# Optimization experiments

Hardware: AMD Instinct MI355X
Metric: run time of the kernel (lower is better)

## Reference

```python
import jax, jax.numpy as jnp
import numpy as np

C = 1.0          # curvature
KP_EXTENT = 0.66 # kernel point influence radius
N, NEI, K, DIN, DOUT = 20000, 16, 4, 64, 64


def _artanh(x):
    return jnp.arctanh(jnp.clip(x, -1.0 + 1e-7, 1.0 - 1e-7))

def _norm(x):
    return jnp.sqrt(jnp.clip(jnp.sum(x * x, -1, keepdims=True), 1e-14))

def _proj(x, c=C):
    n = _norm(x)
    maxn = (1.0 - 1e-5) / jnp.sqrt(c)
    return jnp.where(n > maxn, x / n * maxn, x)

def _expmap0(u, c=C):
    sc = jnp.sqrt(c)
    n = _norm(u)
    return jnp.tanh(sc * n) * u / (sc * n)

def _logmap0(p, c=C):
    sc = jnp.sqrt(c)
    n = _norm(p)
    return _artanh(sc * n) * p / (sc * n)

def _mobius_add(x, y, c=C):
    x2 = jnp.sum(x * x, -1, keepdims=True)
    y2 = jnp.sum(y * y, -1, keepdims=True)
    xy = jnp.sum(x * y, -1, keepdims=True)
    num = (1 + 2 * c * xy + c * y2) * x + (1 - c * x2) * y
    den = jnp.clip(1 + 2 * c * xy + c * c * x2 * y2, 1e-15)
    return num / den

def _lambda_x(x, c=C):
    return 2.0 / jnp.clip(1 - c * jnp.sum(x * x, -1, keepdims=True), 1e-7)

def _dist(x, y, c=C):  # sqrt(sqdist)
    sc = jnp.sqrt(c)
    m = _mobius_add(-x, y, c)
    return (2.0 / sc) * _artanh(sc * _norm(m)[..., 0])

def _logmap(x, y, c=C):
    m = _mobius_add(-x, y, c)
    n = _norm(m)
    sc = jnp.sqrt(c)
    return 2.0 / (sc * _lambda_x(x, c)) * _artanh(sc * n) * m / n

def _ptransp0back(x, u, c=C):  # parallel transport x -> origin
    return u * _lambda_x(x, c) / 2.0

def _p2k(x, c=C):  # Poincare -> Klein
    return 2.0 * x / (1 + c * jnp.sum(x * x, -1, keepdims=True))

def _k2p(x, c=C):  # Klein -> Poincare
    return x / (1 + jnp.sqrt(jnp.clip(1 - c * jnp.sum(x * x, -1, keepdims=True), 1e-7)))

def _gamma(x, c=C):  # Lorentz factor of a Klein point
    return 1.0 / jnp.sqrt(jnp.clip(1 - c * jnp.sum(x * x, -1, keepdims=True), 1e-7))


def setup_inputs() -> dict:
    key = jax.random.key(0)
    k1, k2, k3, k4, k5 = jax.random.split(key, 5)
    x = _proj(0.1 * jax.random.normal(k1, (N, DIN), jnp.float32))   # points in the ball
    nei = jax.random.randint(k2, (N, NEI), 0, N)                    # neighbor indices
    nei_mask = jnp.ones((N, NEI), jnp.float32)
    W = jax.random.normal(k3, (K, DOUT, DIN), jnp.float32) * (2.0 / (DIN + DOUT)) ** 0.5
    b = 0.01 * jax.random.normal(k4, (K, DOUT), jnp.float32)
    kt = jax.random.normal(k5, (K, DIN), jnp.float32)
    kt = kt / _norm(kt) * KP_EXTENT                                 # tangent kernel points on radius
    kt = kt.at[0].set(0.0)                                          # center kernel point
    return {"x": x, "nei": nei, "nei_mask": nei_mask, "W": W, "b": b, "kernel_tangents": kt}


def reference(x, nei, nei_mask, W, b, kernel_tangents):
    # 1) irregular neighbor gather: (N, NEI, D)
    x_nei = x[nei]
    xr = x[:, None, :]
    # 2) transport_x: move every neighborhood to the origin
    x0_nei = _proj(_expmap0(_ptransp0back(xr, _logmap(xr, x_nei))))
    # 3) kernel positions at the origin (after transport, transp=False branch)
    x_kernel = _expmap0(kernel_tangents)                        # (K, D)
    # 4) per neighbor / kernel-point hyperbolic distances: (N, K, NEI)
    dis = _dist(x0_nei[:, None, :, :], x_kernel[None, :, None, :])
    # 5) per-kernel BLinear: log0 -> linear -> exp0 -> mobius bias add -> proj
    u = _logmap0(x0_nei)                                        # (N, NEI, D)
    h = _expmap0(jnp.einsum('kod,bnd->bkno', W, u))             # (N, K, NEI, DOUT)
    h = _proj(_mobius_add(h, _expmap0(b)[None, :, None, :]))
    # 6) KPConv linear influence weights, masked
    w = jax.nn.relu(1.0 - dis / KP_EXTENT) * nei_mask[:, None, :]
    # 7) Klein weighted midpoint over neighbors (AggKlein=True)
    kx = _p2k(h)
    wg = w * _gamma(kx)[..., 0]                                 # (N, K, NEI)
    mid = jnp.einsum('bkn,bknd->bkd', wg, kx) / jnp.clip(jnp.sum(wg, -1, keepdims=True)[..., None][..., 0, :], 1e-10)
    # 8) Klein midpoint over the K kernel points
    g = _gamma(mid)                                             # (N, K, 1)
    out_k = jnp.sum(g * mid, 1) / jnp.clip(jnp.sum(g, 1), 1e-10)
    out = _proj(_k2p(out_k))
    # 9) hyperbolic activation (BAct with relu in tangent space at origin)
    return _expmap0(jax.nn.relu(_logmap0(out)))
```

## Files before the change

kernel.cpp:

```cpp
#include <hip/hip_runtime.h>

#define NEI 16
#define KK 4
#define DIN 64
#define DOUT 64
#define WPB 4
#define BLK (WPB * 64)
#define MAXBLOCKS 2048

__device__ __forceinline__ float wave_bcast_sum(float v) {
#pragma unroll
  for (int s = 1; s < 64; s <<= 1) v += __shfl_xor(v, s, 64);
  return v;
}

__device__ __forceinline__ float artanh_c(float z) {
  z = fminf(z, 1.0f - 1e-7f);
  z = fmaxf(z, -1.0f + 1e-7f);
  return atanhf(z);
}

__device__ __forceinline__ float tanh_fast(float r) {
  const float e = __expf(2.f * r);
  return (e - 1.f) / (e + 1.f);
}

__device__ __forceinline__ float cosh_fast(float t) {
  const float e = __expf(t);
  return 0.5f * (e + 1.f / e);
}

__global__ __launch_bounds__(BLK) void kpa_fused(
    const float* __restrict__ x, const int* __restrict__ nei,
    const float* __restrict__ nmask, const float* __restrict__ Wg,
    const float* __restrict__ bias, const float* __restrict__ kt,
    float* __restrict__ out, int npts) {
  __shared__ __align__(16) float sXK[KK][DIN];
  __shared__ __align__(16) float sEB[KK][DOUT];
  __shared__ float sXK2[KK], sEB2[KK], sAT[KK];
  __shared__ __align__(16) float sUv[WPB][DIN];

  const int tid = threadIdx.x, wv = tid >> 6, lane = tid & 63;

  {
    float v = kt[wv * DIN + lane];
    float bv = bias[wv * DOUT + lane];
    float n2 = wave_bcast_sum(v * v);
    float nr = sqrtf(fmaxf(n2, 1e-14f));
    float t = tanh_fast(nr);
    sXK[wv][lane] = t / nr * v;
    float bn2 = wave_bcast_sum(bv * bv);
    float bnr = sqrtf(fmaxf(bn2, 1e-14f));
    float tb = tanh_fast(bnr);
    sEB[wv][lane] = tb / bnr * bv;
    if (lane == 0) {
      sXK2[wv] = t * t;
      sEB2[wv] = tb * tb;
      sAT[wv] = nr;
    }
  }
  __syncthreads();

  const float maxAT = fmaxf(fmaxf(sAT[0], sAT[1]), fmaxf(sAT[2], sAT[3]));
  const float Cthr = 0.5f * (cosh_fast(0.68f + 2.f * maxAT) - 1.f);

  const int nn = lane >> 2, q = lane & 3, kme = lane & 3;
  const int stride = gridDim.x * WPB;

  int b = blockIdx.x * WPB + wv;
  if (b >= npts) return;

  int jc = nei[b * NEI + nn];
  float4 yc[4], xc[4];
  {
    const float4* yr = reinterpret_cast<const float4*>(x + (size_t)jc * DIN);
    const float4* xr = reinterpret_cast<const float4*>(x + (size_t)b * DIN);
#pragma unroll
    for (int c = 0; c < 4; ++c) {
      xc[c] = xr[c * 4 + q];
      yc[c] = yr[c * 4 + q];
    }
  }
  int b1 = b + stride;
  int j1 = (b1 < npts) ? nei[b1 * NEI + nn] : 0;

  for (;;) {
    const bool hasn = (b1 < npts);

    float4 yn[4], xn[4];
    if (hasn) {
      const float4* yr = reinterpret_cast<const float4*>(x + (size_t)j1 * DIN);
      const float4* xr = reinterpret_cast<const float4*>(x + (size_t)b1 * DIN);
#pragma unroll
      for (int c = 0; c < 4; ++c) {
        xn[c] = xr[c * 4 + q];
        yn[c] = yr[c * 4 + q];
      }
    }
    const int b2 = b1 + stride;
    int j2 = 0;
    if (hasn && b2 < npts) j2 = nei[b2 * NEI + nn];
    __builtin_amdgcn_sched_barrier(0);

    float xyc[4], y2c[4], x2c[4];
#pragma unroll
    for (int c = 0; c < 4; ++c) {
      float a = yc[c].x * xc[c].x, d = yc[c].x * yc[c].x, e = xc[c].x * xc[c].x;
      a = fmaf(yc[c].y, xc[c].y, a); d = fmaf(yc[c].y, yc[c].y, d); e = fmaf(xc[c].y, xc[c].y, e);
      a = fmaf(yc[c].z, xc[c].z, a); d = fmaf(yc[c].z, yc[c].z, d); e = fmaf(xc[c].z, xc[c].z, e);
      a = fmaf(yc[c].w, xc[c].w, a); d = fmaf(yc[c].w, yc[c].w, d); e = fmaf(xc[c].w, xc[c].w, e);
      xyc[c] = a; y2c[c] = d; x2c[c] = e;
    }
    float xy = (xyc[0] + xyc[1]) + (xyc[2] + xyc[3]);
    float y2 = (y2c[0] + y2c[1]) + (y2c[2] + y2c[3]);
    float x2 = (x2c[0] + x2c[1]) + (x2c[2] + x2c[3]);
#pragma unroll
    for (int s = 1; s < 4; s <<= 1) {
      xy += __shfl_xor(xy, s, 64);
      y2 += __shfl_xor(y2, s, 64);
      x2 += __shfl_xor(x2, s, 64);
    }

    const float e2 = fmaxf(x2 - 2.f * xy + y2, 0.f);
    const bool nearp = e2 < Cthr * (1.f - x2) * (1.f - y2);

    if (__ballot(nearp) == 0ull) {
      out[(size_t)b * DOUT + lane] = 0.f;
    } else {
      const float Bc = 1.f - x2;
      const float A = 1.f - 2.f * xy + y2;
      const float den = fmaxf(1.f - 2.f * xy + x2 * y2, 1e-15f);
      const float inv = 1.f / den;
      const float num2 = fmaxf(A * A * x2 - 2.f * A * Bc * xy + Bc * Bc * y2, 0.f);
      const float nm2 = num2 * inv * inv;

      const float mskme = nmask[b * NEI + nn];
      float dk[KK] = {0.f, 0.f, 0.f, 0.f};
      float pk[KK] = {0.f, 0.f, 0.f, 0.f};
#pragma unroll
      for (int k = 0; k < KK; ++k) {
        const float4* xkp = reinterpret_cast<const float4*>(&sXK[k][0]);
#pragma unroll
        for (int c = 0; c < 4; ++c) {
          const float4 xk4 = xkp[c * 4 + q];
          dk[k] = fmaf(yc[c].x, xk4.x, dk[k]); dk[k] = fmaf(yc[c].y, xk4.y, dk[k]);
          dk[k] = fmaf(yc[c].z, xk4.z, dk[k]); dk[k] = fmaf(yc[c].w, xk4.w, dk[k]);
          pk[k] = fmaf(xc[c].x, xk4.x, pk[k]); pk[k] = fmaf(xc[c].y, xk4.y, pk[k]);
          pk[k] = fmaf(xc[c].z, xk4.z, pk[k]); pk[k] = fmaf(xc[c].w, xk4.w, pk[k]);
        }
      }
#pragma unroll
      for (int s = 1; s < 4; s <<= 1) {
#pragma unroll
        for (int k = 0; k < KK; ++k) {
          dk[k] += __shfl_xor(dk[k], s, 64);
          pk[k] += __shfl_xor(pk[k], s, 64);
        }
      }
      const float Pjme = dk[kme];
      const float Pbme = pk[kme];

      const float nmr = sqrtf(fmaxf(nm2, 1e-14f));
      const float scl = (nmr > 0.99999f) ? (0.99999f / nmr) : 1.f;
      const float fac = inv * scl;
      const float n02 = nm2 * scl * scl;
      const float B2 = 1.f - n02;
      const float dd = fac * (Bc * Pjme - A * Pbme);
      const float xk2 = sXK2[kme];
      const float A2 = 1.f - 2.f * dd + xk2;
      const float dn2 = fmaxf(1.f - 2.f * dd + n02 * xk2, 1e-15f);
      const float nu2 = fmaxf(A2 * A2 * n02 - 2.f * A2 * B2 * dd + B2 * B2 * xk2, 0.f);
      const float mm2 = nu2 / (dn2 * dn2);
      float w = 0.f;
      if (mm2 < 0.101505f && mskme > 0.f) {
        const float dis = 2.f * artanh_c(sqrtf(fmaxf(mm2, 1e-14f)));
        w = fmaxf(1.f - dis * (1.0f / 0.66f), 0.f) * mskme;
      }
      const unsigned long long act = __ballot(w > 0.f);
      if (act == 0ull) {
        out[(size_t)b * DOUT + lane] = 0.f;
      } else {
        const float xbd = x[(size_t)b * DIN + lane];
        float midv[KK];
#pragma unroll
        for (int k = 0; k < KK; ++k) {
          float macc = 0.f, wsm = 0.f;
          unsigned long long m = act & (0x1111111111111111ull << k);
          const float ebt = sEB[k][lane];
          const float eb2 = sEB2[k];
          while (m) {
            const int g = __ffsll(m) - 1;
            m &= m - 1;
            const float wn = __shfl(w, g, 64);
            const float fac_n = __shfl(fac, g, 64);
            const float A_n = __shfl(A, g, 64);
            const float n02_n = __shfl(n02, g, 64);
            const int j_n = __shfl(jc, g, 64);
            const float yd = x[(size_t)j_n * DIN + lane];
            const float x0t = fac_n * (Bc * yd - A_n * xbd);
            const float n0 = sqrtf(fmaxf(n02_n, 1e-14f));
            const float al = artanh_c(n0) / n0;
            asm volatile("s_waitcnt lgkmcnt(0)" ::: "memory");
            sUv[wv][lane] = al * x0t;
            asm volatile("s_waitcnt lgkmcnt(0)" ::: "memory");
            __builtin_amdgcn_sched_barrier(0);
            float a0 = 0.f, a1 = 0.f, a2 = 0.f, a3 = 0.f;
            const float4* wrow = reinterpret_cast<const float4*>(Wg) + ((k * DOUT + lane) << 4);
            const float4* urow = reinterpret_cast<const float4*>(&sUv[wv][0]);
#pragma unroll
            for (int g4 = 0; g4 < 16; ++g4) {
              const float4 w4 = wrow[g4];
              const float4 u4 = urow[g4];
              a0 = fmaf(w4.x, u4.x, a0);
              a1 = fmaf(w4.y, u4.y, a1);
              a2 = fmaf(w4.z, u4.z, a2);
              a3 = fmaf(w4.w, u4.w, a3);
            }
            const float hpre = (a0 + a1) + (a2 + a3);
            const float nh2 = wave_bcast_sum(hpre * hpre);
            const float nh = sqrtf(fmaxf(nh2, 1e-14f));
            const float sh = tanhf(nh) / nh;
            const float ht = sh * hpre;
            const float hx2 = sh * sh * nh2;
            const float hxy = wave_bcast_sum(ht * ebt);
            const float A3 = 1.f + 2.f * hxy + eb2;
            const float B3 = 1.f - hx2;
            const float dn3 = fmaxf(1.f + 2.f * hxy + hx2 * eb2, 1e-15f);
            float hm = (A3 * ht + B3 * ebt) / dn3;
            float n2h = wave_bcast_sum(hm * hm);
            const float nnh = sqrtf(fmaxf(n2h, 1e-14f));
            if (nnh > 0.99999f) {
              const float s = 0.99999f / nnh;
              hm *= s;
              n2h *= s * s;
            }
            const float ip = 1.f / (1.f + n2h);
            const float kx = 2.f * hm * ip;
            const float kx2 = 4.f * n2h * ip * ip;
            const float gam = 1.f / sqrtf(fmaxf(1.f - kx2, 1e-7f));
            const float wgv = wn * gam;
            macc = fmaf(wgv, kx, macc);
            wsm += wgv;
          }
          midv[k] = macc / fmaxf(wsm, 1e-10f);
        }

        float m2v[KK];
#pragma unroll
        for (int k = 0; k < KK; ++k) m2v[k] = midv[k] * midv[k];
#pragma unroll
        for (int s = 1; s < 64; s <<= 1) {
#pragma unroll
          for (int k = 0; k < KK; ++k) m2v[k] += __shfl_xor(m2v[k], s, 64);
        }
        float onum = 0.f, oden = 0.f;
#pragma unroll
        for (int k = 0; k < KK; ++k) {
          const float g = 1.f / sqrtf(fmaxf(1.f - m2v[k], 1e-7f));
          onum = fmaf(g, midv[k], onum);
          oden += g;
        }
        const float ok = onum / fmaxf(oden, 1e-10f);
        const float no2 = wave_bcast_sum(ok * ok);
        float p = ok / (1.f + sqrtf(fmaxf(1.f - no2, 1e-7f)));
        float np2 = wave_bcast_sum(p * p);
        float npn = sqrtf(fmaxf(np2, 1e-14f));
        if (npn > 0.99999f) {
          p *= 0.99999f / npn;
          npn = 0.99999f;
        }
        const float al2 = artanh_c(npn) / npn;
        const float rr = fmaxf(al2 * p, 0.f);
        const float nr2 = wave_bcast_sum(rr * rr);
        const float nrr = sqrtf(fmaxf(nr2, 1e-14f));
        out[(size_t)b * DOUT + lane] = tanhf(nrr) / nrr * rr;
      }
    }

    if (!hasn) break;
    b = b1;
    jc = j1;
    b1 = b2;
    j1 = j2;
#pragma unroll
    for (int c = 0; c < 4; ++c) {
      yc[c] = yn[c];
      xc[c] = xn[c];
    }
  }
}

extern "C" void kernel_launch(void* const* d_in, const int* in_sizes, int n_in,
                              void* d_out, int out_size, void* d_ws, size_t ws_size,
                              hipStream_t stream) {
  const float* x = (const float*)d_in[0];
  const int* nei = (const int*)d_in[1];
  const float* nmask = (const float*)d_in[2];
  const float* W = (const float*)d_in[3];
  const float* bias = (const float*)d_in[4];
  const float* kt = (const float*)d_in[5];
  float* out = (float*)d_out;

  const int npts = in_sizes[0] / DIN;
  int grid = (npts + WPB - 1) / WPB;
  if (grid > MAXBLOCKS) grid = MAXBLOCKS;
  kpa_fused<<<grid, BLK, 0, stream>>>(x, nei, nmask, W, bias, kt, out, npts);
}
```

Before: 23.33 us.

## Split into gate kernel building a worklist and a compact heavy kernel

Adds a light gate kernel that zeroes every output row, runs the cheap proximity test per point, and appends surviving point indices to a workspace worklist through an atomic counter. A second kernel with a fixed grid of 128 blocks then processes only the listed points with the full hyperbolic pipeline. The aim is to remove divergence and the idle slots that sparse active points leave in the grid-stride fused loop. In exchange it adds a memset and an extra launch, plus atomic contention. The fused kernel is kept as a fallback when no workspace is available, and its register prefetch pipelining is removed.

```diff
diff --git a/kernel.cpp b/kernel.cpp
--- a/kernel.cpp
+++ b/kernel.cpp
@@ -7,6 +7,7 @@
 #define WPB 4
 #define BLK (WPB * 64)
 #define MAXBLOCKS 2048
+#define WLOFF 64
 
 __device__ __forceinline__ float wave_bcast_sum(float v) {
 #pragma unroll
@@ -28,6 +29,265 @@
 __device__ __forceinline__ float cosh_fast(float t) {
   const float e = __expf(t);
   return 0.5f * (e + 1.f / e);
+}
+
+__global__ __launch_bounds__(BLK, 6) void kpa_gate(
+    const float* __restrict__ x, const int* __restrict__ nei,
+    const float* __restrict__ kt, float* __restrict__ out,
+    int* __restrict__ wl, int npts) {
+  __shared__ float sAT[KK];
+  const int tid = threadIdx.x, wv = tid >> 6, lane = tid & 63;
+  {
+    float v = kt[wv * DIN + lane];
+    float n2 = wave_bcast_sum(v * v);
+    if (lane == 0) sAT[wv] = sqrtf(fmaxf(n2, 1e-14f));
+  }
+  __syncthreads();
+  const float maxAT = fmaxf(fmaxf(sAT[0], sAT[1]), fmaxf(sAT[2], sAT[3]));
+  const float Cthr = 0.5f * (cosh_fast(0.68f + 2.f * maxAT) - 1.f);
+
+  const int b = blockIdx.x * WPB + wv;
+  if (b >= npts) return;
+  const int nn = lane >> 2, q = lane & 3;
+  const int j = nei[b * NEI + nn];
+
+  out[(size_t)b * DOUT + lane] = 0.f;
+
+  const float4* yr = reinterpret_cast<const float4*>(x + (size_t)j * DIN);
+  const float4* xr = reinterpret_cast<const float4*>(x + (size_t)b * DIN);
+  float xy = 0.f, y2 = 0.f, x2 = 0.f;
+#pragma unroll
+  for (int c = 0; c < 4; ++c) {
+    const float4 yv = yr[c * 4 + q];
+    const float4 xv = xr[c * 4 + q];
+    xy = fmaf(yv.x, xv.x, xy); xy = fmaf(yv.y, xv.y, xy);
+    xy = fmaf(yv.z, xv.z, xy); xy = fmaf(yv.w, xv.w, xy);
+    y2 = fmaf(yv.x, yv.x, y2); y2 = fmaf(yv.y, yv.y, y2);
+    y2 = fmaf(yv.z, yv.z, y2); y2 = fmaf(yv.w, yv.w, y2);
+    x2 = fmaf(xv.x, xv.x, x2); x2 = fmaf(xv.y, xv.y, x2);
+    x2 = fmaf(xv.z, xv.z, x2); x2 = fmaf(xv.w, xv.w, x2);
+  }
+#pragma unroll
+  for (int s = 1; s < 4; s <<= 1) {
+    xy += __shfl_xor(xy, s, 64);
+    y2 += __shfl_xor(y2, s, 64);
+    x2 += __shfl_xor(x2, s, 64);
+  }
+  const float e2 = fmaxf(x2 - 2.f * xy + y2, 0.f);
+  const bool nearp = e2 < Cthr * (1.f - x2) * (1.f - y2);
+  if (__ballot(nearp) != 0ull && lane == 0) {
+    const int idx = atomicAdd(wl, 1);
+    wl[WLOFF + idx] = b;
+  }
+}
+
+__global__ __launch_bounds__(BLK) void kpa_heavy(
+    const float* __restrict__ x, const int* __restrict__ nei,
+    const float* __restrict__ nmask, const float* __restrict__ Wg,
+    const float* __restrict__ bias, const float* __restrict__ kt,
+    const int* __restrict__ wl, float* __restrict__ out, int npts) {
+  __shared__ __align__(16) float sXK[KK][DIN];
+  __shared__ __align__(16) float sEB[KK][DOUT];
+  __shared__ float sXK2[KK], sEB2[KK];
+  __shared__ __align__(16) float sUv[WPB][DIN];
+
+  const int tid = threadIdx.x, wv = tid >> 6, lane = tid & 63;
+  {
+    float v = kt[wv * DIN + lane];
+    float bv = bias[wv * DOUT + lane];
+    float n2 = wave_bcast_sum(v * v);
+    float nr = sqrtf(fmaxf(n2, 1e-14f));
+    float t = tanh_fast(nr);
+    sXK[wv][lane] = t / nr * v;
+    float bn2 = wave_bcast_sum(bv * bv);
+    float bnr = sqrtf(fmaxf(bn2, 1e-14f));
+    float tb = tanh_fast(bnr);
+    sEB[wv][lane] = tb / bnr * bv;
+    if (lane == 0) {
+      sXK2[wv] = t * t;
+      sEB2[wv] = tb * tb;
+    }
+  }
+  __syncthreads();
+
+  const int cnt = wl[0];
+  const int nn = lane >> 2, q = lane & 3, kme = lane & 3;
+  const int stride = gridDim.x * WPB;
+
+  for (int i = blockIdx.x * WPB + wv; i < cnt; i += stride) {
+    const int b = wl[WLOFF + i];
+    const int jc = nei[b * NEI + nn];
+    const float mskme = nmask[b * NEI + nn];
+
+    float4 yc[4], xc[4];
+    {
+      const float4* yr = reinterpret_cast<const float4*>(x + (size_t)jc * DIN);
+      const float4* xr = reinterpret_cast<const float4*>(x + (size_t)b * DIN);
+#pragma unroll
+      for (int c = 0; c < 4; ++c) {
+        xc[c] = xr[c * 4 + q];
+        yc[c] = yr[c * 4 + q];
+      }
+    }
+    float xy = 0.f, y2 = 0.f, x2 = 0.f;
+    float dk[KK] = {0.f, 0.f, 0.f, 0.f};
+    float pk[KK] = {0.f, 0.f, 0.f, 0.f};
+#pragma unroll
+    for (int c = 0; c < 4; ++c) {
+      xy = fmaf(yc[c].x, xc[c].x, xy); xy = fmaf(yc[c].y, xc[c].y, xy);
+      xy = fmaf(yc[c].z, xc[c].z, xy); xy = fmaf(yc[c].w, xc[c].w, xy);
+      y2 = fmaf(yc[c].x, yc[c].x, y2); y2 = fmaf(yc[c].y, yc[c].y, y2);
+      y2 = fmaf(yc[c].z, yc[c].z, y2); y2 = fmaf(yc[c].w, yc[c].w, y2);
+      x2 = fmaf(xc[c].x, xc[c].x, x2); x2 = fmaf(xc[c].y, xc[c].y, x2);
+      x2 = fmaf(xc[c].z, xc[c].z, x2); x2 = fmaf(xc[c].w, xc[c].w, x2);
+    }
+#pragma unroll
+    for (int k = 0; k < KK; ++k) {
+      const float4* xkp = reinterpret_cast<const float4*>(&sXK[k][0]);
+#pragma unroll
+      for (int c = 0; c < 4; ++c) {
+        const float4 xk4 = xkp[c * 4 + q];
+        dk[k] = fmaf(yc[c].x, xk4.x, dk[k]); dk[k] = fmaf(yc[c].y, xk4.y, dk[k]);
+        dk[k] = fmaf(yc[c].z, xk4.z, dk[k]); dk[k] = fmaf(yc[c].w, xk4.w, dk[k]);
+        pk[k] = fmaf(xc[c].x, xk4.x, pk[k]); pk[k] = fmaf(xc[c].y, xk4.y, pk[k]);
+        pk[k] = fmaf(xc[c].z, xk4.z, pk[k]); pk[k] = fmaf(xc[c].w, xk4.w, pk[k]);
+      }
+    }
+#pragma unroll
+    for (int s = 1; s < 4; s <<= 1) {
+      xy += __shfl_xor(xy, s, 64);
+      y2 += __shfl_xor(y2, s, 64);
+      x2 += __shfl_xor(x2, s, 64);
+#pragma unroll
+      for (int k = 0; k < KK; ++k) {
+        dk[k] += __shfl_xor(dk[k], s, 64);
+        pk[k] += __shfl_xor(pk[k], s, 64);
+      }
+    }
+
+    const float Bc = 1.f - x2;
+    const float A = 1.f - 2.f * xy + y2;
+    const float den = fmaxf(1.f - 2.f * xy + x2 * y2, 1e-15f);
+    const float inv = 1.f / den;
+    const float num2 = fmaxf(A * A * x2 - 2.f * A * Bc * xy + Bc * Bc * y2, 0.f);
+    const float nm2 = num2 * inv * inv;
+    const float nmr = sqrtf(fmaxf(nm2, 1e-14f));
+    const float scl = (nmr > 0.99999f) ? (0.99999f / nmr) : 1.f;
+    const float fac = inv * scl;
+    const float n02 = nm2 * scl * scl;
+    const float B2 = 1.f - n02;
+    const float dd = fac * (Bc * dk[kme] - A * pk[kme]);
+    const float xk2 = sXK2[kme];
+    const float A2 = 1.f - 2.f * dd + xk2;
+    const float dn2 = fmaxf(1.f - 2.f * dd + n02 * xk2, 1e-15f);
+    const float nu2 = fmaxf(A2 * A2 * n02 - 2.f * A2 * B2 * dd + B2 * B2 * xk2, 0.f);
+    const float mm2 = nu2 / (dn2 * dn2);
+    float w = 0.f;
+    if (mm2 < 0.101505f && mskme > 0.f) {
+      const float dis = 2.f * artanh_c(sqrtf(fmaxf(mm2, 1e-14f)));
+      w = fmaxf(1.f - dis * (1.0f / 0.66f), 0.f) * mskme;
+    }
+    const unsigned long long act = __ballot(w > 0.f);
+    if (act == 0ull) {
+      out[(size_t)b * DOUT + lane] = 0.f;
+      continue;
+    }
+
+    const float xbd = x[(size_t)b * DIN + lane];
+    float midv[KK];
+#pragma unroll
+    for (int k = 0; k < KK; ++k) {
+      float macc = 0.f, wsm = 0.f;
+      unsigned long long m = act & (0x1111111111111111ull << k);
+      const float ebt = sEB[k][lane];
+      const float eb2 = sEB2[k];
+      while (m) {
+        const int g = __ffsll(m) - 1;
+        m &= m - 1;
+        const float wn = __shfl(w, g, 64);
+        const float fac_n = __shfl(fac, g, 64);
+        const float A_n = __shfl(A, g, 64);
+        const float n02_n = __shfl(n02, g, 64);
+        const int j_n = __shfl(jc, g, 64);
+        const float yd = x[(size_t)j_n * DIN + lane];
+        const float x0t = fac_n * (Bc * yd - A_n * xbd);
+        const float n0 = sqrtf(fmaxf(n02_n, 1e-14f));
+        const float al = artanh_c(n0) / n0;
+        asm volatile("s_waitcnt lgkmcnt(0)" ::: "memory");
+        sUv[wv][lane] = al * x0t;
+        asm volatile("s_waitcnt lgkmcnt(0)" ::: "memory");
+        __builtin_amdgcn_sched_barrier(0);
+        float a0 = 0.f, a1 = 0.f, a2 = 0.f, a3 = 0.f;
+        const float4* wrow = reinterpret_cast<const float4*>(Wg) + ((k * DOUT + lane) << 4);
+        const float4* urow = reinterpret_cast<const float4*>(&sUv[wv][0]);
+#pragma unroll
+        for (int g4 = 0; g4 < 16; ++g4) {
+          const float4 w4 = wrow[g4];
+          const float4 u4 = urow[g4];
+          a0 = fmaf(w4.x, u4.x, a0);
+          a1 = fmaf(w4.y, u4.y, a1);
+          a2 = fmaf(w4.z, u4.z, a2);
+          a3 = fmaf(w4.w, u4.w, a3);
+        }
+        const float hpre = (a0 + a1) + (a2 + a3);
+        const float nh2 = wave_bcast_sum(hpre * hpre);
+        const float nh = sqrtf(fmaxf(nh2, 1e-14f));
+        const float sh = tanhf(nh) / nh;
+        const float ht = sh * hpre;
+        const float hx2 = sh * sh * nh2;
+        const float hxy = wave_bcast_sum(ht * ebt);
+        const float A3 = 1.f + 2.f * hxy + eb2;
+        const float B3 = 1.f - hx2;
+        const float dn3 = fmaxf(1.f + 2.f * hxy + hx2 * eb2, 1e-15f);
+        float hm = (A3 * ht + B3 * ebt) / dn3;
+        float n2h = wave_bcast_sum(hm * hm);
+        const float nnh = sqrtf(fmaxf(n2h, 1e-14f));
+        if (nnh > 0.99999f) {
+          const float s = 0.99999f / nnh;
+          hm *= s;
+          n2h *= s * s;
+        }
+        const float ip = 1.f / (1.f + n2h);
+        const float kx = 2.f * hm * ip;
+        const float kx2 = 4.f * n2h * ip * ip;
+        const float gam = 1.f / sqrtf(fmaxf(1.f - kx2, 1e-7f));
+        const float wgv = wn * gam;
+        macc = fmaf(wgv, kx, macc);
+        wsm += wgv;
+      }
+      midv[k] = macc / fmaxf(wsm, 1e-10f);
+    }
+
+    float m2v[KK];
+#pragma unroll
+    for (int k = 0; k < KK; ++k) m2v[k] = midv[k] * midv[k];
+#pragma unroll
+    for (int s = 1; s < 64; s <<= 1) {
+#pragma unroll
+      for (int k = 0; k < KK; ++k) m2v[k] += __shfl_xor(m2v[k], s, 64);
+    }
+    float onum = 0.f, oden = 0.f;
+#pragma unroll
+    for (int k = 0; k < KK; ++k) {
+      const float g = 1.f / sqrtf(fmaxf(1.f - m2v[k], 1e-7f));
+      onum = fmaf(g, midv[k], onum);
+      oden += g;
+    }
+    const float ok = onum / fmaxf(oden, 1e-10f);
+    const float no2 = wave_bcast_sum(ok * ok);
+    float p = ok / (1.f + sqrtf(fmaxf(1.f - no2, 1e-7f)));
+    float np2 = wave_bcast_sum(p * p);
+    float npn = sqrtf(fmaxf(np2, 1e-14f));
+    if (npn > 0.99999f) {
+      p *= 0.99999f / npn;
+      npn = 0.99999f;
+    }
+    const float al2 = artanh_c(npn) / npn;
+    const float rr = fmaxf(al2 * p, 0.f);
+    const float nr2 = wave_bcast_sum(rr * rr);
+    const float nrr = sqrtf(fmaxf(nr2, 1e-14f));
+    out[(size_t)b * DOUT + lane] = tanhf(nrr) / nrr * rr;
+  }
 }
 
 __global__ __launch_bounds__(BLK) void kpa_fused(
@@ -41,7 +301,6 @@
   __shared__ __align__(16) float sUv[WPB][DIN];
 
   const int tid = threadIdx.x, wv = tid >> 6, lane = tid & 63;
-
   {
     float v = kt[wv * DIN + lane];
     float bv = bias[wv * DOUT + lane];
@@ -63,230 +322,186 @@
 
   const float maxAT = fmaxf(fmaxf(sAT[0], sAT[1]), fmaxf(sAT[2], sAT[3]));
   const float Cthr = 0.5f * (cosh_fast(0.68f + 2.f * maxAT) - 1.f);
-
   const int nn = lane >> 2, q = lane & 3, kme = lane & 3;
   const int stride = gridDim.x * WPB;
 
-  int b = blockIdx.x * WPB + wv;
-  if (b >= npts) return;
-
-  int jc = nei[b * NEI + nn];
-  float4 yc[4], xc[4];
-  {
-    const float4* yr = reinterpret_cast<const float4*>(x + (size_t)jc * DIN);
-    const float4* xr = reinterpret_cast<const float4*>(x + (size_t)b * DIN);
+  for (int b = blockIdx.x * WPB + wv; b < npts; b += stride) {
+    const int jc = nei[b * NEI + nn];
+    float4 yc[4], xc[4];
+    {
+      const float4* yr = reinterpret_cast<const float4*>(x + (size_t)jc * DIN);
+      const float4* xr = reinterpret_cast<const float4*>(x + (size_t)b * DIN);
+#pragma unroll
+      for (int c = 0; c < 4; ++c) {
+        xc[c] = xr[c * 4 + q];
+        yc[c] = yr[c * 4 + q];
+      }
+    }
+    float xy = 0.f, y2 = 0.f, x2 = 0.f;
 #pragma unroll
     for (int c = 0; c < 4; ++c) {
-      xc[c] = xr[c * 4 + q];
-      yc[c] = yr[c * 4 + q];
-    }
-  }
-  int b1 = b + stride;
-  int j1 = (b1 < npts) ? nei[b1 * NEI + nn] : 0;
-
-  for (;;) {
-    const bool hasn = (b1 < npts);
-
-    float4 yn[4], xn[4];
-    if (hasn) {
-      const float4* yr = reinterpret_cast<const float4*>(x + (size_t)j1 * DIN);
-      const float4* xr = reinterpret_cast<const float4*>(x + (size_t)b1 * DIN);
-#pragma unroll
-      for (int c = 0; c < 4; ++c) {
-        xn[c] = xr[c * 4 + q];
-        yn[c] = yr[c * 4 + q];
-      }
-    }
-    const int b2 = b1 + stride;
-    int j2 = 0;
-    if (hasn && b2 < npts) j2 = nei[b2 * NEI + nn];
-    __builtin_amdgcn_sched_barrier(0);
-
-    float xyc[4], y2c[4], x2c[4];
-#pragma unroll
-    for (int c = 0; c < 4; ++c) {
-      float a = yc[c].x * xc[c].x, d = yc[c].x * yc[c].x, e = xc[c].x * xc[c].x;
-      a = fmaf(yc[c].y, xc[c].y, a); d = fmaf(yc[c].y, yc[c].y, d); e = fmaf(xc[c].y, xc[c].y, e);
-      a = fmaf(yc[c].z, xc[c].z, a); d = fmaf(yc[c].z, yc[c].z, d); e = fmaf(xc[c].z, xc[c].z, e);
-      a = fmaf(yc[c].w, xc[c].w, a); d = fmaf(yc[c].w, yc[c].w, d); e = fmaf(xc[c].w, xc[c].w, e);
-      xyc[c] = a; y2c[c] = d; x2c[c] = e;
-    }
-    float xy = (xyc[0] + xyc[1]) + (xyc[2] + xyc[3]);
-    float y2 = (y2c[0] + y2c[1]) + (y2c[2] + y2c[3]);
-    float x2 = (x2c[0] + x2c[1]) + (x2c[2] + x2c[3]);
+      xy = fmaf(yc[c].x, xc[c].x, xy); xy = fmaf(yc[c].y, xc[c].y, xy);
+      xy = fmaf(yc[c].z, xc[c].z, xy); xy = fmaf(yc[c].w, xc[c].w, xy);
+      y2 = fmaf(yc[c].x, yc[c].x, y2); y2 = fmaf(yc[c].y, yc[c].y, y2);
+      y2 = fmaf(yc[c].z, yc[c].z, y2); y2 = fmaf(yc[c].w, yc[c].w, y2);
+      x2 = fmaf(xc[c].x, xc[c].x, x2); x2 = fmaf(xc[c].y, xc[c].y, x2);
+      x2 = fmaf(xc[c].w, xc[c].w, x2); x2 = fmaf(xc[c].z, xc[c].z, x2);
+    }
 #pragma unroll
     for (int s = 1; s < 4; s <<= 1) {
       xy += __shfl_xor(xy, s, 64);
       y2 += __shfl_xor(y2, s, 64);
       x2 += __shfl_xor(x2, s, 64);
     }
-
     const float e2 = fmaxf(x2 - 2.f * xy + y2, 0.f);
     const bool nearp = e2 < Cthr * (1.f - x2) * (1.f - y2);
-
     if (__ballot(nearp) == 0ull) {
       out[(size_t)b * DOUT + lane] = 0.f;
-    } else {
-      const float Bc = 1.f - x2;
-      const float A = 1.f - 2.f * xy + y2;
-      const float den = fmaxf(1.f - 2.f * xy + x2 * y2, 1e-15f);
-      const float inv = 1.f / den;
-      const float num2 = fmaxf(A * A * x2 - 2.f * A * Bc * xy + Bc * Bc * y2, 0.f);
-      const float nm2 = num2 * inv * inv;
-
-      const float mskme = nmask[b * NEI + nn];
-      float dk[KK] = {0.f, 0.f, 0.f, 0.f};
-      float pk[KK] = {0.f, 0.f, 0.f, 0.f};
+      continue;
+    }
+    const float Bc = 1.f - x2;
+    const float A = 1.f - 2.f * xy + y2;
+    const float den = fmaxf(1.f - 2.f * xy + x2 * y2, 1e-15f);
+    const float inv = 1.f / den;
+    const float num2 = fmaxf(A * A * x2 - 2.f * A * Bc * xy + Bc * Bc * y2, 0.f);
+    const float nm2 = num2 * inv * inv;
+    const float mskme = nmask[b * NEI + nn];
+    float dk[KK] = {0.f, 0.f, 0.f, 0.f};
+    float pk[KK] = {0.f, 0.f, 0.f, 0.f};
+#pragma unroll
+    for (int k = 0; k < KK; ++k) {
+      const float4* xkp = reinterpret_cast<const float4*>(&sXK[k][0]);
+#pragma unroll
+      for (int c = 0; c < 4; ++c) {
+        const float4 xk4 = xkp[c * 4 + q];
+        dk[k] = fmaf(yc[c].x, xk4.x, dk[k]); dk[k] = fmaf(yc[c].y, xk4.y, dk[k]);
+        dk[k] = fmaf(yc[c].z, xk4.z, dk[k]); dk[k] = fmaf(yc[c].w, xk4.w, dk[k]);
+        pk[k] = fmaf(xc[c].x, xk4.x, pk[k]); pk[k] = fmaf(xc[c].y, xk4.y, pk[k]);
+        pk[k] = fmaf(xc[c].z, xk4.z, pk[k]); pk[k] = fmaf(xc[c].w, xk4.w, pk[k]);
+      }
+    }
+#pragma unroll
+    for (int s = 1; s < 4; s <<= 1) {
 #pragma unroll
       for (int k = 0; k < KK; ++k) {
-        const float4* xkp = reinterpret_cast<const float4*>(&sXK[k][0]);
-#pragma unroll
-        for (int c = 0; c < 4; ++c) {
-          const float4 xk4 = xkp[c * 4 + q];
-          dk[k] = fmaf(yc[c].x, xk4.x, dk[k]); dk[k] = fmaf(yc[c].y, xk4.y, dk[k]);
-          dk[k] = fmaf(yc[c].z, xk4.z, dk[k]); dk[k] = fmaf(yc[c].w, xk4.w, dk[k]);
-          pk[k] = fmaf(xc[c].x, xk4.x, pk[k]); pk[k] = fmaf(xc[c].y, xk4.y, pk[k]);
-          pk[k] = fmaf(xc[c].z, xk4.z, pk[k]); pk[k] = fmaf(xc[c].w, xk4.w, pk[k]);
+        dk[k] += __shfl_xor(dk[k], s, 64);
+        pk[k] += __shfl_xor(pk[k], s, 64);
+      }
+    }
+    const float nmr = sqrtf(fmaxf(nm2, 1e-14f));
+    const float scl = (nmr > 0.99999f) ? (0.99999f / nmr) : 1.f;
+    const float fac = inv * scl;
+    const float n02 = nm2 * scl * scl;
+    const float B2 = 1.f - n02;
+    const float dd = fac * (Bc * dk[kme] - A * pk[kme]);
+    const float xk2 = sXK2[kme];
+    const float A2 = 1.f - 2.f * dd + xk2;
+    const float dn2 = fmaxf(1.f - 2.f * dd + n02 * xk2, 1e-15f);
+    const float nu2 = fmaxf(A2 * A2 * n02 - 2.f * A2 * B2 * dd + B2 * B2 * xk2, 0.f);
+    const float mm2 = nu2 / (dn2 * dn2);
+    float w = 0.f;
+    if (mm2 < 0.101505f && mskme > 0.f) {
+      const float dis = 2.f * artanh_c(sqrtf(fmaxf(mm2, 1e-14f)));
+      w = fmaxf(1.f - dis * (1.0f / 0.66f), 0.f) * mskme;
+    }
+    const unsigned long long act = __ballot(w > 0.f);
+    if (act == 0ull) {
+      out[(size_t)b * DOUT + lane] = 0.f;
+      continue;
+    }
+    const float xbd = x[(size_t)b * DIN + lane];
+    float midv[KK];
+#pragma unroll
+    for (int k = 0; k < KK; ++k) {
+      float macc = 0.f, wsm = 0.f;
+      unsigned long long m = act & (0x1111111111111111ull << k);
+      const float ebt = sEB[k][lane];
+      const float eb2 = sEB2[k];
+      while (m) {
+        const int g = __ffsll(m) - 1;
+        m &= m - 1;
+        const float wn = __shfl(w, g, 64);
+        const float fac_n = __shfl(fac, g, 64);
+        const float A_n = __shfl(A, g, 64);
+        const float n02_n = __shfl(n02, g, 64);
+        const int j_n = __shfl(jc, g, 64);
+        const float yd = x[(size_t)j_n * DIN + lane];
+        const float x0t = fac_n * (Bc * yd - A_n * xbd);
+        const float n0 = sqrtf(fmaxf(n02_n, 1e-14f));
+        const float al = artanh_c(n0) / n0;
+        asm volatile("s_waitcnt lgkmcnt(0)" ::: "memory");
+        sUv[wv][lane] = al * x0t;
+        asm volatile("s_waitcnt lgkmcnt(0)" ::: "memory");
+        __builtin_amdgcn_sched_barrier(0);
+        float a0 = 0.f, a1 = 0.f, a2 = 0.f, a3 = 0.f;
+        const float4* wrow = reinterpret_cast<const float4*>(Wg) + ((k * DOUT + lane) << 4);
+        const float4* urow = reinterpret_cast<const float4*>(&sUv[wv][0]);
+#pragma unroll
+        for (int g4 = 0; g4 < 16; ++g4) {
+          const float4 w4 = wrow[g4];
+          const float4 u4 = urow[g4];
+          a0 = fmaf(w4.x, u4.x, a0);
+          a1 = fmaf(w4.y, u4.y, a1);
+          a2 = fmaf(w4.z, u4.z, a2);
+          a3 = fmaf(w4.w, u4.w, a3);
         }
-      }
-#pragma unroll
-      for (int s = 1; s < 4; s <<= 1) {
-#pragma unroll
-        for (int k = 0; k < KK; ++k) {
-          dk[k] += __shfl_xor(dk[k], s, 64);
-          pk[k] += __shfl_xor(pk[k], s, 64);
+        const float hpre = (a0 + a1) + (a2 + a3);
+        const float nh2 = wave_bcast_sum(hpre * hpre);
+        const float nh = sqrtf(fmaxf(nh2, 1e-14f));
+        const float sh = tanhf(nh) / nh;
+        const float ht = sh * hpre;
+        const float hx2 = sh * sh * nh2;
+        const float hxy = wave_bcast_sum(ht * ebt);
+        const float A3 = 1.f + 2.f * hxy + eb2;
+        const float B3 = 1.f - hx2;
+        const float dn3 = fmaxf(1.f + 2.f * hxy + hx2 * eb2, 1e-15f);
+        float hm = (A3 * ht + B3 * ebt) / dn3;
+        float n2h = wave_bcast_sum(hm * hm);
+        const float nnh = sqrtf(fmaxf(n2h, 1e-14f));
+        if (nnh > 0.99999f) {
+          const float s = 0.99999f / nnh;
+          hm *= s;
+          n2h *= s * s;
         }
-      }
-      const float Pjme = dk[kme];
-      const float Pbme = pk[kme];
-
-      const float nmr = sqrtf(fmaxf(nm2, 1e-14f));
-      const float scl = (nmr > 0.99999f) ? (0.99999f / nmr) : 1.f;
-      const float fac = inv * scl;
-      const float n02 = nm2 * scl * scl;
-      const float B2 = 1.f - n02;
-      const float dd = fac * (Bc * Pjme - A * Pbme);
-      const float xk2 = sXK2[kme];
-      const float A2 = 1.f - 2.f * dd + xk2;
-      const float dn2 = fmaxf(1.f - 2.f * dd + n02 * xk2, 1e-15f);
-      const float nu2 = fmaxf(A2 * A2 * n02 - 2.f * A2 * B2 * dd + B2 * B2 * xk2, 0.f);
-      const float mm2 = nu2 / (dn2 * dn2);
-      float w = 0.f;
-      if (mm2 < 0.101505f && mskme > 0.f) {
-        const float dis = 2.f * artanh_c(sqrtf(fmaxf(mm2, 1e-14f)));
-        w = fmaxf(1.f - dis * (1.0f / 0.66f), 0.f) * mskme;
-      }
-      const unsigned long long act = __ballot(w > 0.f);
-      if (act == 0ull) {
-        out[(size_t)b * DOUT + lane] = 0.f;
-      } else {
-        const float xbd = x[(size_t)b * DIN + lane];
-        float midv[KK];
-#pragma unroll
-        for (int k = 0; k < KK; ++k) {
-          float macc = 0.f, wsm = 0.f;
-          unsigned long long m = act & (0x1111111111111111ull << k);
-          const float ebt = sEB[k][lane];
-          const float eb2 = sEB2[k];
-          while (m) {
-            const int g = __ffsll(m) - 1;
-            m &= m - 1;
-            const float wn = __shfl(w, g, 64);
-            const float fac_n = __shfl(fac, g, 64);
-            const float A_n = __shfl(A, g, 64);
-            const float n02_n = __shfl(n02, g, 64);
-            const int j_n = __shfl(jc, g, 64);
-            const float yd = x[(size_t)j_n * DIN + lane];
-            const float x0t = fac_n * (Bc * yd - A_n * xbd);
-            const float n0 = sqrtf(fmaxf(n02_n, 1e-14f));
-            const float al = artanh_c(n0) / n0;
-            asm volatile("s_waitcnt lgkmcnt(0)" ::: "memory");
-            sUv[wv][lane] = al * x0t;
-            asm volatile("s_waitcnt lgkmcnt(0)" ::: "memory");
-            __builtin_amdgcn_sched_barrier(0);
-            float a0 = 0.f, a1 = 0.f, a2 = 0.f, a3 = 0.f;
-            const float4* wrow = reinterpret_cast<const float4*>(Wg) + ((k * DOUT + lane) << 4);
-            const float4* urow = reinterpret_cast<const float4*>(&sUv[wv][0]);
-#pragma unroll
-            for (int g4 = 0; g4 < 16; ++g4) {
-              const float4 w4 = wrow[g4];
-              const float4 u4 = urow[g4];
-              a0 = fmaf(w4.x, u4.x, a0);
-              a1 = fmaf(w4.y, u4.y, a1);
-              a2 = fmaf(w4.z, u4.z, a2);
-              a3 = fmaf(w4.w, u4.w, a3);
-            }
-            const float hpre = (a0 + a1) + (a2 + a3);
-            const float nh2 = wave_bcast_sum(hpre * hpre);
-            const float nh = sqrtf(fmaxf(nh2, 1e-14f));
-            const float sh = tanhf(nh) / nh;
-            const float ht = sh * hpre;
-            const float hx2 = sh * sh * nh2;
-            const float hxy = wave_bcast_sum(ht * ebt);
-            const float A3 = 1.f + 2.f * hxy + eb2;
-            const float B3 = 1.f - hx2;
-            const float dn3 = fmaxf(1.f + 2.f * hxy + hx2 * eb2, 1e-15f);
-            float hm = (A3 * ht + B3 * ebt) / dn3;
-            float n2h = wave_bcast_sum(hm * hm);
-            const float nnh = sqrtf(fmaxf(n2h, 1e-14f));
-            if (nnh > 0.99999f) {
-              const float s = 0.99999f / nnh;
-              hm *= s;
-              n2h *= s * s;
-            }
-            const float ip = 1.f / (1.f + n2h);
-            const float kx = 2.f * hm * ip;
-            const float kx2 = 4.f * n2h * ip * ip;
-            const float gam = 1.f / sqrtf(fmaxf(1.f - kx2, 1e-7f));
-            const float wgv = wn * gam;
-            macc = fmaf(wgv, kx, macc);
-            wsm += wgv;
-          }
-          midv[k] = macc / fmaxf(wsm, 1e-10f);
-        }
-
-        float m2v[KK];
-#pragma unroll
-        for (int k = 0; k < KK; ++k) m2v[k] = midv[k] * midv[k];
-#pragma unroll
-        for (int s = 1; s < 64; s <<= 1) {
-#pragma unroll
-          for (int k = 0; k < KK; ++k) m2v[k] += __shfl_xor(m2v[k], s, 64);
-        }
-        float onum = 0.f, oden = 0.f;
-#pragma unroll
-        for (int k = 0; k < KK; ++k) {
-          const float g = 1.f / sqrtf(fmaxf(1.f - m2v[k], 1e-7f));
-          onum = fmaf(g, midv[k], onum);
-          oden += g;
-        }
-        const float ok = onum / fmaxf(oden, 1e-10f);
-        const float no2 = wave_bcast_sum(ok * ok);
-        float p = ok / (1.f + sqrtf(fmaxf(1.f - no2, 1e-7f)));
-        float np2 = wave_bcast_sum(p * p);
-        float npn = sqrtf(fmaxf(np2, 1e-14f));
-        if (npn > 0.99999f) {
-          p *= 0.99999f / npn;
-          npn = 0.99999f;
-        }
-        const float al2 = artanh_c(npn) / npn;
-        const float rr = fmaxf(al2 * p, 0.f);
-        const float nr2 = wave_bcast_sum(rr * rr);
-        const float nrr = sqrtf(fmaxf(nr2, 1e-14f));
-        out[(size_t)b * DOUT + lane] = tanhf(nrr) / nrr * rr;
-      }
-    }
-
-    if (!hasn) break;
-    b = b1;
-    jc = j1;
-    b1 = b2;
-    j1 = j2;
-#pragma unroll
-    for (int c = 0; c < 4; ++c) {
-      yc[c] = yn[c];
-      xc[c] = xn[c];
-    }
+        const float ip = 1.f / (1.f + n2h);
+        const float kx = 2.f * hm * ip;
+        const float kx2 = 4.f * n2h * ip * ip;
+        const float gam = 1.f / sqrtf(fmaxf(1.f - kx2, 1e-7f));
+        const float wgv = wn * gam;
+        macc = fmaf(wgv, kx, macc);
+        wsm += wgv;
+      }
+      midv[k] = macc / fmaxf(wsm, 1e-10f);
+    }
+    float m2v[KK];
+#pragma unroll
+    for (int k = 0; k < KK; ++k) m2v[k] = midv[k] * midv[k];
+#pragma unroll
+    for (int s = 1; s < 64; s <<= 1) {
+#pragma unroll
+      for (int k = 0; k < KK; ++k) m2v[k] += __shfl_xor(m2v[k], s, 64);
+    }
+    float onum = 0.f, oden = 0.f;
+#pragma unroll
+    for (int k = 0; k < KK; ++k) {
+      const float g = 1.f / sqrtf(fmaxf(1.f - m2v[k], 1e-7f));
+      onum = fmaf(g, midv[k], onum);
+      oden += g;
+    }
+    const float ok = onum / fmaxf(oden, 1e-10f);
+    const float no2 = wave_bcast_sum(ok * ok);
+    float p = ok / (1.f + sqrtf(fmaxf(1.f - no2, 1e-7f)));
+    float np2 = wave_bcast_sum(p * p);
+    float npn = sqrtf(fmaxf(np2, 1e-14f));
+    if (npn > 0.99999f) {
+      p *= 0.99999f / npn;
+      npn = 0.99999f;
+    }
+    const float al2 = artanh_c(npn) / npn;
+    const float rr = fmaxf(al2 * p, 0.f);
+    const float nr2 = wave_bcast_sum(rr * rr);
+    const float nrr = sqrtf(fmaxf(nr2, 1e-14f));
+    out[(size_t)b * DOUT + lane] = tanhf(nrr) / nrr * rr;
   }
 }
 
@@ -302,7 +517,17 @@
   float* out = (float*)d_out;
 
   const int npts = in_sizes[0] / DIN;
-  int grid = (npts + WPB - 1) / WPB;
-  if (grid > MAXBLOCKS) grid = MAXBLOCKS;
-  kpa_fused<<<grid, BLK, 0, stream>>>(x, nei, nmask, W, bias, kt, out, npts);
-}
+  const size_t need = ((size_t)WLOFF + (size_t)npts) * sizeof(int);
+
+  if (d_ws != nullptr && ws_size >= need) {
+    int* wl = (int*)d_ws;
+    hipMemsetAsync(wl, 0, sizeof(int), stream);
+    const int gridA = (npts + WPB - 1) / WPB;
+    kpa_gate<<<gridA, BLK, 0, stream>>>(x, nei, kt, out, wl, npts);
+    kpa_heavy<<<128, BLK, 0, stream>>>(x, nei, nmask, W, bias, kt, wl, out, npts);
+  } else {
+    int grid = (npts + WPB - 1) / WPB;
+    if (grid > MAXBLOCKS) grid = MAXBLOCKS;
+    kpa_fused<<<grid, BLK, 0, stream>>>(x, nei, nmask, W, bias, kt, out, npts);
+  }
+}
```

Result: slower. 29.04 us (+24.5%).
